# Kernel optimization log

Measured on AMD Instinct MI355X. Metric: run time of the kernel, lower is better.

Reference implementation:

```python
import jax, jax.numpy as jnp
import numpy as np

NUM_HEADS = 16
D_MODEL = 1024
DEPTH = D_MODEL // NUM_HEADS
THRESHOLD = 0.1
BATCH = 2
SEQ = 2048


def setup_inputs() -> dict:
    key = jax.random.key(0)
    ks = jax.random.split(key, 9)
    w_scale = 1.0 / np.sqrt(D_MODEL)
    Q = jax.random.normal(ks[0], (BATCH, SEQ, D_MODEL), dtype=jnp.float32)
    T = jax.random.normal(ks[1], (BATCH, SEQ, D_MODEL), dtype=jnp.float32)
    V = jax.random.normal(ks[2], (BATCH, SEQ, D_MODEL), dtype=jnp.float32)
    Wq = jax.random.normal(ks[3], (NUM_HEADS, D_MODEL, DEPTH), dtype=jnp.float32) * w_scale
    Wk = jax.random.normal(ks[4], (NUM_HEADS, D_MODEL, DEPTH), dtype=jnp.float32) * w_scale
    Wv = jax.random.normal(ks[5], (NUM_HEADS, D_MODEL, DEPTH), dtype=jnp.float32) * w_scale
    Wo = jax.random.normal(ks[6], (D_MODEL, D_MODEL), dtype=jnp.float32) * w_scale
    bq = jnp.zeros((NUM_HEADS, DEPTH), dtype=jnp.float32)
    bk = jnp.zeros((NUM_HEADS, DEPTH), dtype=jnp.float32)
    bv = jnp.zeros((NUM_HEADS, DEPTH), dtype=jnp.float32)
    bo = jnp.zeros((D_MODEL,), dtype=jnp.float32)
    return {"Q": Q, "T": T, "V": V, "Wq": Wq, "bq": bq, "Wk": Wk, "bk": bk,
            "Wv": Wv, "bv": bv, "Wo": Wo, "bo": bo}


def reference(Q, T, V, Wq, bq, Wk, bk, Wv, bv, Wo, bo):
    # Per-head projections (stacked over heads): [B,S,D] x [H,D,E] -> [B,H,S,E]
    q = jnp.einsum('bsd,hde->bhse', Q, Wq) + bq[None, :, None, :]
    k = jnp.einsum('bsd,hde->bhse', T, Wk) + bk[None, :, None, :]
    v = jnp.einsum('bsd,hde->bhse', V, Wv) + bv[None, :, None, :]

    # Raw scores (NOT pre-scaled): [B,H,S,S]
    scores = jnp.einsum('bhqe,bhke->bhqk', q, k)
    # tf.where(A>thr, A, -2**32 * cast(A>thr)) -> failing entries become 0
    scores = jnp.where(scores > THRESHOLD, scores, jnp.zeros((), scores.dtype))
    # M = 1 - lower_band(ones): +1 on strictly upper-triangular entries
    seq = scores.shape[-1]
    upper = jnp.triu(jnp.ones((seq, seq), dtype=scores.dtype), k=1)
    scores = (scores + upper) / jnp.sqrt(jnp.asarray(DEPTH, scores.dtype))

    attn = jax.nn.softmax(scores, axis=-1)
    out = jnp.einsum('bhqk,bhke->bhqe', attn, v)  # [B,H,S,E]
    B, H, S, E = out.shape
    concat = out.transpose(0, 2, 1, 3).reshape(B, S, H * E)  # [B,S,D]
    return concat @ Wo + bo
```

## Files before the change

### kernel.cpp

```cpp
#include <hip/hip_runtime.h>
#include <stdint.h>


typedef __attribute__((ext_vector_type(8))) short bf16x8;
typedef __attribute__((ext_vector_type(4))) float f32x4;

#define DEVFN static __device__ __forceinline__

static constexpr int S_ = 2048;
static constexpr int H_ = 16;

DEVFN unsigned short f2bf(float x) {
  union { float f; uint32_t u; } v; v.f = x;
  const uint32_t r = v.u + 0x7fffu + ((v.u >> 16) & 1u);
  return (unsigned short)(r >> 16);
}

DEVFN f32x4 fzero() { f32x4 v = {0.f, 0.f, 0.f, 0.f}; return v; }

union U8 { uint32_t u[4]; bf16x8 v; };

DEVFN void gld_lds16(const void* g, void* lds) {
  __builtin_amdgcn_global_load_lds(
      (const __attribute__((address_space(1))) void*)g,
      (__attribute__((address_space(3))) void*)lds, 16, 0, 0);
}

__global__ void prep_weights(const float* __restrict__ Wq, const float* __restrict__ Wk,
                             const float* __restrict__ Wv, const float* __restrict__ Wo,
                             unsigned short* __restrict__ dstBase) {
  const int z = blockIdx.z;
  const float* src = (z == 0) ? Wq : (z == 1) ? Wk : (z == 2) ? Wv : Wo;
  unsigned short* dst = dstBase + (size_t)z * (1024u * 1024u);
  const int idx = blockIdx.x * 256 + threadIdx.x;
  const int c = idx & 1023;
  const int d0 = (idx >> 10) << 3;
  unsigned short hv[8];
#pragma unroll
  for (int t = 0; t < 8; ++t) {
    const int d = d0 + t;
    const float v = (z < 3) ? src[(size_t)((c >> 6) * 1024 + d) * 64 + (c & 63)]
                            : src[(size_t)d * 1024 + c];
    hv[t] = f2bf(v);
  }
  *(uint4*)(dst + (size_t)c * 1024 + d0) = *(const uint4*)hv;
}

__global__ __launch_bounds__(256, 3)
void proj_gemm(const float* __restrict__ Qm, const float* __restrict__ Tm,
               const float* __restrict__ Vm, const unsigned short* __restrict__ Wt,
               const float* __restrict__ bq, const float* __restrict__ bk,
               const float* __restrict__ bv, unsigned short* __restrict__ qb,
               unsigned short* __restrict__ kb, unsigned short* __restrict__ vtb) {
  __shared__ float Af[2][128 * 32];
  __shared__ unsigned short Bt[2][128 * 32];

  const int tid = threadIdx.x;
  const int lane = tid & 63;
  const int w = tid >> 6;
  const int g = lane >> 4, c = lane & 15;
  const int wm = w >> 1, wn = w & 1;

  const int orig = blockIdx.x;
  const int xcd = orig & 7;
  const int l = orig >> 3;
  const int bx = xcd * 4 + l / 24;
  const int by = l % 24;

  const int m0 = bx * 128;
  const int proj = by >> 3;
  const int n0 = (by & 7) * 128;

  const float* Asrc = (proj == 0) ? Qm : (proj == 1) ? Tm : Vm;
  const unsigned short* W = Wt + (size_t)proj * (1024u * 1024u);

  f32x4 acc[4][4];
#pragma unroll
  for (int i = 0; i < 4; ++i)
#pragma unroll
    for (int j = 0; j < 4; ++j) acc[i][j] = fzero();

  const int arow = w * 8 + (lane >> 3);
  const int ach = lane & 7;
  const int brow = w * 16 + (lane >> 2);
  const int bch = lane & 3;

  auto stage = [&](int kt, int buf) {
#pragma unroll
    for (int u = 0; u < 4; ++u) {
      const int row = u * 32 + arow;
      const int ch = ach ^ (row & 7);
      gld_lds16(Asrc + (size_t)(m0 + row) * 1024 + kt * 32 + ch * 4,
                &Af[buf][(u * 32 + w * 8) * 32]);
    }
#pragma unroll
    for (int u = 0; u < 2; ++u) {
      const int row = u * 64 + brow;
      const int ch = bch ^ ((row >> 1) & 3);
      gld_lds16(W + (size_t)(n0 + row) * 1024 + kt * 32 + ch * 8,
                &Bt[buf][(u * 64 + w * 16) * 32]);
    }
  };

  stage(0, 0);
  __syncthreads();

  for (int kt = 0; kt < 32; ++kt) {
    const int buf = kt & 1;
    if (kt < 31) stage(kt + 1, buf ^ 1);

    bf16x8 af[4], bfr[4];
#pragma unroll
    for (int mi = 0; mi < 4; ++mi) {
      const int row = wm * 64 + mi * 16 + c;
      const int swz = row & 7;
      const float4 fa = *(const float4*)&Af[buf][row * 32 + ((2 * g) ^ swz) * 4];
      const float4 fb = *(const float4*)&Af[buf][row * 32 + ((2 * g + 1) ^ swz) * 4];
      U8 u8;
      asm("v_cvt_pk_bf16_f32 %0, %1, %2" : "=v"(u8.u[0]) : "v"(fa.x), "v"(fa.y));
      asm("v_cvt_pk_bf16_f32 %0, %1, %2" : "=v"(u8.u[1]) : "v"(fa.z), "v"(fa.w));
      asm("v_cvt_pk_bf16_f32 %0, %1, %2" : "=v"(u8.u[2]) : "v"(fb.x), "v"(fb.y));
      asm("v_cvt_pk_bf16_f32 %0, %1, %2" : "=v"(u8.u[3]) : "v"(fb.z), "v"(fb.w));
      af[mi] = u8.v;
    }
#pragma unroll
    for (int ni = 0; ni < 4; ++ni) {
      const int row = wn * 64 + ni * 16 + c;
      bfr[ni] = *(const bf16x8*)&Bt[buf][row * 32 + ((g ^ ((row >> 1) & 3))) * 8];
    }
#pragma unroll
    for (int mi = 0; mi < 4; ++mi)
#pragma unroll
      for (int ni = 0; ni < 4; ++ni)
        acc[mi][ni] = __builtin_amdgcn_mfma_f32_16x16x32_bf16(af[mi], bfr[ni],
                                                              acc[mi][ni], 0, 0, 0);
    __syncthreads();
  }

  const float* bias = (proj == 0) ? bq : (proj == 1) ? bk : bv;
  if (proj < 2) {
    unsigned short* dptr = (proj == 0) ? qb : kb;
#pragma unroll
    for (int ni = 0; ni < 4; ++ni) {
      const int colb = n0 + wn * 64 + ni * 16 + c;
      const float bc = bias[colb];
      const int hh = colb >> 6, e = colb & 63;
#pragma unroll
      for (int mi = 0; mi < 4; ++mi)
#pragma unroll
        for (int r = 0; r < 4; ++r) {
          const int row = m0 + wm * 64 + mi * 16 + g * 4 + r;
          const int bb = row >> 11, s = row & 2047;
          dptr[(((size_t)(bb * H_ + hh)) * S_ + s) * 64 + e] = f2bf(acc[mi][ni][r] + bc);
        }
    }
  } else {
#pragma unroll
    for (int ni = 0; ni < 4; ++ni) {
      const int colb = n0 + wn * 64 + ni * 16 + c;
      const float bc = bias[colb];
      const int hh = colb >> 6, e = colb & 63;
#pragma unroll
      for (int mi = 0; mi < 4; ++mi) {
        const int rowb = m0 + wm * 64 + mi * 16 + g * 4;
        const int bb = rowb >> 11, s0 = rowb & 2047;
        const float v0 = acc[mi][ni][0] + bc, v1 = acc[mi][ni][1] + bc;
        const float v2 = acc[mi][ni][2] + bc, v3 = acc[mi][ni][3] + bc;
        uint2 pk;
        asm("v_cvt_pk_bf16_f32 %0, %1, %2" : "=v"(pk.x) : "v"(v0), "v"(v1));
        asm("v_cvt_pk_bf16_f32 %0, %1, %2" : "=v"(pk.y) : "v"(v2), "v"(v3));
        *(uint2*)&vtb[(((size_t)(bb * H_ + hh)) * 64 + e) * S_ + s0] = pk;
      }
    }
  }
}

__global__ __launch_bounds__(256, 2)
void attn_kernel(const unsigned short* __restrict__ qb,
                 const unsigned short* __restrict__ kb,
                 const unsigned short* __restrict__ vtb,
                 unsigned short* __restrict__ att) {
  __shared__ unsigned short Kt[2][128 * 64];
  __shared__ unsigned short Vt[2][64 * 128];
  __shared__ unsigned short Pt[4][32 * 64];

  const int tid = threadIdx.x;
  const int lane = tid & 63;
  const int w = tid >> 6;
  const int g = lane >> 4, c = lane & 15;

  const int orig = blockIdx.x;
  const int logical = ((orig & 7) << 6) | (orig >> 3);
  const int qblk = logical & 15;
  const int bh = logical >> 4;
  const int hh = bh & 15, bz = bh >> 4;

  const int q0w = qblk * 128 + w * 32;
  const unsigned short* qh = qb + (size_t)bh * S_ * 64;
  const unsigned short* kh = kb + (size_t)bh * S_ * 64;
  const unsigned short* vh = vtb + (size_t)bh * 64 * S_;

  bf16x8 aq[2][2];
#pragma unroll
  for (int m = 0; m < 2; ++m)
#pragma unroll
    for (int t = 0; t < 2; ++t)
      aq[m][t] = *(const bf16x8*)&qh[(size_t)(q0w + m * 16 + c) * 64 + t * 32 + g * 8];

  bf16x8 onesB;
#pragma unroll
  for (int i = 0; i < 8; ++i) onesB[i] = (short)0x3F80;

  f32x4 O[2][4];
  f32x4 accL[2];
#pragma unroll
  for (int m = 0; m < 2; ++m) {
#pragma unroll
    for (int ne = 0; ne < 4; ++ne) O[m][ne] = fzero();
    accL[m] = fzero();
  }

  constexpr float L2E = 1.4426950408889634f;
  const float S2 = 0.125f * L2E;
  const float B2 = 0.125f * L2E;

  int kaOff[2][4];
  int vOff[2][2][4];
  int paOff[2][2], pwOff[2][4];
#pragma unroll
  for (int ks = 0; ks < 2; ++ks) {
#pragma unroll
    for (int mi = 0; mi < 4; ++mi) {
      const int row = mi * 16 + c;
      kaOff[ks][mi] = 2 * (row * 64 + ((ks * 4 + g) ^ (row & 7)) * 8);
    }
#pragma unroll
    for (int m = 0; m < 2; ++m)
      paOff[m][ks] = 2 * ((m * 16 + c) * 64 + ((ks * 4 + g) ^ (c & 7)) * 8);
  }
#pragma unroll
  for (int s = 0; s < 2; ++s)
#pragma unroll
    for (int ks = 0; ks < 2; ++ks)
#pragma unroll
      for (int ne = 0; ne < 4; ++ne) {
        const int e = ne * 16 + c;
        vOff[s][ks][ne] = 2 * (e * 128 + ((s * 8 + ks * 4 + g) ^ c) * 8);
      }
#pragma unroll
  for (int m = 0; m < 2; ++m)
#pragma unroll
    for (int mi = 0; mi < 4; ++mi)
      pwOff[m][mi] =
          2 * ((m * 16 + c) * 64 + ((2 * mi + (g >> 1)) ^ (c & 7)) * 8 + (g & 1) * 4);

  const int srowK = w * 8 + (lane >> 3);
  const int schK = (lane & 7) ^ (srowK & 7);
  const unsigned short* kS = kh + (size_t)srowK * 64 + schK * 8;
  const int rowV = w * 4 + (lane >> 4);
  const int jV = (lane & 15) ^ rowV;
  const unsigned short* vS = vh + (size_t)rowV * S_ + jV * 8;

  {
#pragma unroll
    for (int u = 0; u < 4; ++u) {
      gld_lds16(kS + u * 2048, &Kt[0][(u * 32 + w * 8) * 64]);
      gld_lds16(vS + (size_t)u * 32768, &Vt[0][(u * 16 + w * 4) * 128]);
    }
  }
  __syncthreads();

#define ATTN_SUB(J0S, SB, CUR)                                                 \
  do {                                                                         \
    const int j0 = (J0S);                                                      \
    f32x4 sa[2][4];                                                            \
    _Pragma("unroll")                                                          \
    for (int m = 0; m < 2; ++m)                                                \
      _Pragma("unroll")                                                        \
      for (int mi = 0; mi < 4; ++mi) sa[m][mi] = fzero();                      \
    __builtin_amdgcn_s_setprio(1);                                             \
    _Pragma("unroll")                                                          \
    for (int ks = 0; ks < 2; ++ks)                                             \
      _Pragma("unroll")                                                        \
      for (int mi = 0; mi < 4; ++mi) {                                         \
        const bf16x8 ka = *(const bf16x8*)((const char*)&Kt[CUR][0] +          \
                                           (SB) * 8192 + kaOff[ks][mi]);       \
        sa[0][mi] = __builtin_amdgcn_mfma_f32_16x16x32_bf16(ka, aq[0][ks],     \
                                                            sa[0][mi], 0, 0, 0);\
        sa[1][mi] = __builtin_amdgcn_mfma_f32_16x16x32_bf16(ka, aq[1][ks],     \
                                                            sa[1][mi], 0, 0, 0);\
      }                                                                        \
    __builtin_amdgcn_s_setprio(0);                                             \
    const bool allUp = (j0 >= q0w + 32);                                       \
    const bool noneUp = (j0 + 63 <= q0w);                                      \
    _Pragma("unroll")                                                          \
    for (int m = 0; m < 2; ++m) {                                              \
      const int iq = q0w + m * 16 + c;                                         \
      _Pragma("unroll")                                                        \
      for (int mi = 0; mi < 4; ++mi) {                                         \
        float pv[4];                                                           \
        if (allUp || noneUp) {                                                 \
          const float bb = allUp ? B2 : 0.f;                                   \
          _Pragma("unroll")                                                    \
          for (int r = 0; r < 4; ++r) {                                        \
            const float v = sa[m][mi][r];                                      \
            pv[r] = __builtin_amdgcn_exp2f(                                    \
                (v > 0.1f) ? __builtin_fmaf(v, S2, bb) : bb);                  \
          }                                                                    \
        } else {                                                               \
          _Pragma("unroll")                                                    \
          for (int r = 0; r < 4; ++r) {                                        \
            const float v = sa[m][mi][r];                                      \
            const float bb = (j0 + mi * 16 + g * 4 + r > iq) ? B2 : 0.f;       \
            pv[r] = __builtin_amdgcn_exp2f(                                    \
                (v > 0.1f) ? __builtin_fmaf(v, S2, bb) : bb);                  \
          }                                                                    \
        }                                                                      \
        uint2 d;                                                               \
        asm("v_cvt_pk_bf16_f32 %0, %1, %2"                                     \
            : "=v"(d.x) : "v"(pv[0]), "v"(pv[1]));                             \
        asm("v_cvt_pk_bf16_f32 %0, %1, %2"                                     \
            : "=v"(d.y) : "v"(pv[2]), "v"(pv[3]));                             \
        *(uint2*)((char*)&Pt[w][0] + pwOff[m][mi]) = d;                        \
      }                                                                        \
    }                                                                          \
    asm volatile("s_waitcnt lgkmcnt(0)" ::: "memory");                         \
    __builtin_amdgcn_sched_barrier(0);                                         \
    __builtin_amdgcn_s_setprio(1);                                             \
    _Pragma("unroll")                                                          \
    for (int ks = 0; ks < 2; ++ks) {                                           \
      const bf16x8 pa0 =                                                       \
          *(const bf16x8*)((const char*)&Pt[w][0] + paOff[0][ks]);             \
      const bf16x8 pa1 =                                                       \
          *(const bf16x8*)((const char*)&Pt[w][0] + paOff[1][ks]);             \
      accL[0] = __builtin_amdgcn_mfma_f32_16x16x32_bf16(pa0, onesB, accL[0],   \
                                                        0, 0, 0);              \
      accL[1] = __builtin_amdgcn_mfma_f32_16x16x32_bf16(pa1, onesB, accL[1],   \
                                                        0, 0, 0);              \
      _Pragma("unroll")                                                        \
      for (int ne = 0; ne < 4; ++ne) {                                         \
        const bf16x8 bv8 = *(const bf16x8*)((const char*)&Vt[CUR][0] +         \
                                            vOff[SB][ks][ne]);                 \
        O[0][ne] = __builtin_amdgcn_mfma_f32_16x16x32_bf16(pa0, bv8, O[0][ne], \
                                                           0, 0, 0);           \
        O[1][ne] = __builtin_amdgcn_mfma_f32_16x16x32_bf16(pa1, bv8, O[1][ne], \
                                                           0, 0, 0);           \
      }                                                                        \
    }                                                                          \
    __builtin_amdgcn_s_setprio(0);                                             \
  } while (0)

#define ATTN_TILE(T, CUR)                                                      \
  do {                                                                         \
    if ((T) < 15) {       \
      _Pragma("unroll")                                                        \
      for (int u = 0; u < 4; ++u) {                                            \
        gld_lds16(kS + 8192 + u * 2048, &Kt[CUR ^ 1][(u * 32 + w * 8) * 64]);  \
        gld_lds16(vS + 128 + (size_t)u * 32768,                                \
                  &Vt[CUR ^ 1][(u * 16 + w * 4) * 128]);                       \
      }                                                                        \
      kS += 8192; vS += 128;                                                   \
    }                                                                          \
    ATTN_SUB((T) * 128, 0, CUR);                                               \
    ATTN_SUB((T) * 128 + 64, 1, CUR);                                          \
    __syncthreads();         \
  } while (0)

  for (int T = 0; T < 16; T += 2) {
    ATTN_TILE(T, 0);
    ATTN_TILE(T + 1, 1);
  }
#undef ATTN_TILE
#undef ATTN_SUB

#pragma unroll
  for (int m = 0; m < 2; ++m)
#pragma unroll
    for (int r = 0; r < 4; ++r) {
      const float il = 1.f / accL[m][r];
      const int qg = q0w + m * 16 + g * 4 + r;
      const size_t ro = ((size_t)(bz * S_ + qg)) * 1024 + hh * 64;
#pragma unroll
      for (int ne = 0; ne < 4; ++ne)
        att[ro + ne * 16 + c] = f2bf(O[m][ne][r] * il);
    }
}

__global__ __launch_bounds__(256, 3)
void out_gemm(const unsigned short* __restrict__ att,
              const unsigned short* __restrict__ WoT,
              const float* __restrict__ bo, float* __restrict__ outp) {
  __shared__ unsigned short At[2][128 * 32];
  __shared__ unsigned short Bt[2][128 * 32];

  const int tid = threadIdx.x;
  const int lane = tid & 63;
  const int w = tid >> 6;
  const int g = lane >> 4, c = lane & 15;
  const int wm = w >> 1, wn = w & 1;

  const int orig = blockIdx.x;
  const int xcd = orig & 7;
  const int l = orig >> 3;
  const int bx = xcd * 4 + l / 8;
  const int by = l % 8;
  const int m0 = bx * 128;
  const int n0 = by * 128;

  f32x4 acc[4][4];
#pragma unroll
  for (int i = 0; i < 4; ++i)
#pragma unroll
    for (int j = 0; j < 4; ++j) acc[i][j] = fzero();

  const int srow = lane >> 2;
  const int sch = lane & 3;

  auto stage = [&](int kt, int buf) {
#pragma unroll
    for (int u = 0; u < 2; ++u) {
      const int row = u * 64 + w * 16 + srow;
      const int ch = sch ^ ((row >> 1) & 3);
      gld_lds16(att + (size_t)(m0 + row) * 1024 + kt * 32 + ch * 8,
                &At[buf][(u * 64 + w * 16) * 32]);
      gld_lds16(WoT + (size_t)(n0 + row) * 1024 + kt * 32 + ch * 8,
                &Bt[buf][(u * 64 + w * 16) * 32]);
    }
  };

  stage(0, 0);
  __syncthreads();

  for (int kt = 0; kt < 32; ++kt) {
    const int buf = kt & 1;
    if (kt < 31) stage(kt + 1, buf ^ 1);

    bf16x8 af[4], bfr[4];
#pragma unroll
    for (int mi = 0; mi < 4; ++mi) {
      const int row = wm * 64 + mi * 16 + c;
      af[mi] = *(const bf16x8*)&At[buf][row * 32 + ((g ^ ((row >> 1) & 3))) * 8];
    }
#pragma unroll
    for (int ni = 0; ni < 4; ++ni) {
      const int row = wn * 64 + ni * 16 + c;
      bfr[ni] = *(const bf16x8*)&Bt[buf][row * 32 + ((g ^ ((row >> 1) & 3))) * 8];
    }
#pragma unroll
    for (int mi = 0; mi < 4; ++mi)
#pragma unroll
      for (int ni = 0; ni < 4; ++ni)
        acc[mi][ni] = __builtin_amdgcn_mfma_f32_16x16x32_bf16(af[mi], bfr[ni],
                                                              acc[mi][ni], 0, 0, 0);
    __syncthreads();
  }

#pragma unroll
  for (int ni = 0; ni < 4; ++ni) {
    const int colb = n0 + wn * 64 + ni * 16 + c;
    const float bc = bo[colb];
#pragma unroll
    for (int mi = 0; mi < 4; ++mi)
#pragma unroll
      for (int r = 0; r < 4; ++r) {
        const int row = m0 + wm * 64 + mi * 16 + g * 4 + r;
        outp[(size_t)row * 1024 + colb] = acc[mi][ni][r] + bc;
      }
  }
}

extern "C" void kernel_launch(void* const* d_in, const int* in_sizes, int n_in,
                              void* d_out, int out_size, void* d_ws, size_t ws_size,
                              hipStream_t stream) {
  const float* Q  = (const float*)d_in[0];
  const float* T  = (const float*)d_in[1];
  const float* V  = (const float*)d_in[2];
  const float* Wq = (const float*)d_in[3];
  const float* bq = (const float*)d_in[4];
  const float* Wk = (const float*)d_in[5];
  const float* bk = (const float*)d_in[6];
  const float* Wv = (const float*)d_in[7];
  const float* bv = (const float*)d_in[8];
  const float* Wo = (const float*)d_in[9];
  const float* bo = (const float*)d_in[10];

  const size_t MB = 1024ull * 1024ull;
  if (ws_size < 40 * MB) return;

  uint8_t* ws = (uint8_t*)d_ws;
  unsigned short* Wt  = (unsigned short*)(ws);
  unsigned short* qb  = (unsigned short*)(ws + 8 * MB);
  unsigned short* kb  = (unsigned short*)(ws + 16 * MB);
  unsigned short* vtb = (unsigned short*)(ws + 24 * MB);
  unsigned short* attb = (unsigned short*)(ws + 32 * MB);

  prep_weights<<<dim3(512, 1, 4), 256, 0, stream>>>(Wq, Wk, Wv, Wo, Wt);
  proj_gemm<<<dim3(768), 256, 0, stream>>>(Q, T, V, Wt, bq, bk, bv,
                                           qb, kb, vtb);
  attn_kernel<<<dim3(512), 256, 0, stream>>>(qb, kb, vtb, attb);
  out_gemm<<<dim3(256), 256, 0, stream>>>(attb, Wt + 3ull * 1024ull * 1024ull,
                                          bo, (float*)d_out);
}
```

Before: 131.5 us.

## Pre-convert projection activations to bf16 in a separate kernel before GEMM

New measurement: 138.3 us. +5.2%, slower.

```diff
diff --git a/kernel.cpp b/kernel.cpp
--- a/kernel.cpp
+++ b/kernel.cpp
@@ -17,8 +17,6 @@
 }
 
 DEVFN f32x4 fzero() { f32x4 v = {0.f, 0.f, 0.f, 0.f}; return v; }
-
-union U8 { uint32_t u[4]; bf16x8 v; };
 
 DEVFN void gld_lds16(const void* g, void* lds) {
   __builtin_amdgcn_global_load_lds(
@@ -46,13 +44,39 @@
   *(uint4*)(dst + (size_t)c * 1024 + d0) = *(const uint4*)hv;
 }
 
-__global__ __launch_bounds__(256, 3)
-void proj_gemm(const float* __restrict__ Qm, const float* __restrict__ Tm,
-               const float* __restrict__ Vm, const unsigned short* __restrict__ Wt,
+__global__ void convert_a(const float* __restrict__ Qm, const float* __restrict__ Tm,
+                          const float* __restrict__ Vm, unsigned short* __restrict__ aq,
+                          unsigned short* __restrict__ at2, unsigned short* __restrict__ av) {
+  const int z = blockIdx.z;
+  const float* s = (z == 0) ? Qm : (z == 1) ? Tm : Vm;
+  unsigned short* d = (z == 0) ? aq : (z == 1) ? at2 : av;
+  const int orig = blockIdx.x;
+  const int xcd = orig & 7;
+  const int j = orig >> 3;
+  const int p = xcd * 4 + (j >> 6);
+  const int inner = j & 63;
+  const size_t i = (size_t)p * 131072 + (size_t)inner * 2048 +
+                   (size_t)threadIdx.x * 8;
+  const float4 f0 = *(const float4*)(s + i);
+  const float4 f1 = *(const float4*)(s + i + 4);
+  uint32_t d0, d1, d2, d3;
+  asm("v_cvt_pk_bf16_f32 %0, %1, %2" : "=v"(d0) : "v"(f0.x), "v"(f0.y));
+  asm("v_cvt_pk_bf16_f32 %0, %1, %2" : "=v"(d1) : "v"(f0.z), "v"(f0.w));
+  asm("v_cvt_pk_bf16_f32 %0, %1, %2" : "=v"(d2) : "v"(f1.x), "v"(f1.y));
+  asm("v_cvt_pk_bf16_f32 %0, %1, %2" : "=v"(d3) : "v"(f1.z), "v"(f1.w));
+  uint4 o; o.x = d0; o.y = d1; o.z = d2; o.w = d3;
+  *(uint4*)(d + i) = o;
+}
+
+__global__ __launch_bounds__(256, 4)
+void proj_gemm(const unsigned short* __restrict__ Aq,
+               const unsigned short* __restrict__ At2,
+               const unsigned short* __restrict__ Av,
+               const unsigned short* __restrict__ Wt,
                const float* __restrict__ bq, const float* __restrict__ bk,
                const float* __restrict__ bv, unsigned short* __restrict__ qb,
                unsigned short* __restrict__ kb, unsigned short* __restrict__ vtb) {
-  __shared__ float Af[2][128 * 32];
+  __shared__ unsigned short At[2][128 * 32];
   __shared__ unsigned short Bt[2][128 * 32];
 
   const int tid = threadIdx.x;
@@ -71,7 +95,7 @@
   const int proj = by >> 3;
   const int n0 = (by & 7) * 128;
 
-  const float* Asrc = (proj == 0) ? Qm : (proj == 1) ? Tm : Vm;
+  const unsigned short* Abf = (proj == 0) ? Aq : (proj == 1) ? At2 : Av;
   const unsigned short* W = Wt + (size_t)proj * (1024u * 1024u);
 
   f32x4 acc[4][4];
@@ -80,23 +104,16 @@
 #pragma unroll
     for (int j = 0; j < 4; ++j) acc[i][j] = fzero();
 
-  const int arow = w * 8 + (lane >> 3);
-  const int ach = lane & 7;
-  const int brow = w * 16 + (lane >> 2);
-  const int bch = lane & 3;
+  const int srow = lane >> 2;
+  const int sch = lane & 3;
 
   auto stage = [&](int kt, int buf) {
 #pragma unroll
-    for (int u = 0; u < 4; ++u) {
-      const int row = u * 32 + arow;
-      const int ch = ach ^ (row & 7);
-      gld_lds16(Asrc + (size_t)(m0 + row) * 1024 + kt * 32 + ch * 4,
-                &Af[buf][(u * 32 + w * 8) * 32]);
-    }
-#pragma unroll
     for (int u = 0; u < 2; ++u) {
-      const int row = u * 64 + brow;
-      const int ch = bch ^ ((row >> 1) & 3);
+      const int row = u * 64 + w * 16 + srow;
+      const int ch = sch ^ ((row >> 1) & 3);
+      gld_lds16(Abf + (size_t)(m0 + row) * 1024 + kt * 32 + ch * 8,
+                &At[buf][(u * 64 + w * 16) * 32]);
       gld_lds16(W + (size_t)(n0 + row) * 1024 + kt * 32 + ch * 8,
                 &Bt[buf][(u * 64 + w * 16) * 32]);
     }
@@ -113,27 +130,21 @@
 #pragma unroll
     for (int mi = 0; mi < 4; ++mi) {
       const int row = wm * 64 + mi * 16 + c;
-      const int swz = row & 7;
-      const float4 fa = *(const float4*)&Af[buf][row * 32 + ((2 * g) ^ swz) * 4];
-      const float4 fb = *(const float4*)&Af[buf][row * 32 + ((2 * g + 1) ^ swz) * 4];
-      U8 u8;
-      asm("v_cvt_pk_bf16_f32 %0, %1, %2" : "=v"(u8.u[0]) : "v"(fa.x), "v"(fa.y));
-      asm("v_cvt_pk_bf16_f32 %0, %1, %2" : "=v"(u8.u[1]) : "v"(fa.z), "v"(fa.w));
-      asm("v_cvt_pk_bf16_f32 %0, %1, %2" : "=v"(u8.u[2]) : "v"(fb.x), "v"(fb.y));
-      asm("v_cvt_pk_bf16_f32 %0, %1, %2" : "=v"(u8.u[3]) : "v"(fb.z), "v"(fb.w));
-      af[mi] = u8.v;
+      af[mi] = *(const bf16x8*)&At[buf][row * 32 + ((g ^ ((row >> 1) & 3))) * 8];
     }
 #pragma unroll
     for (int ni = 0; ni < 4; ++ni) {
       const int row = wn * 64 + ni * 16 + c;
       bfr[ni] = *(const bf16x8*)&Bt[buf][row * 32 + ((g ^ ((row >> 1) & 3))) * 8];
     }
+    __builtin_amdgcn_s_setprio(1);
 #pragma unroll
     for (int mi = 0; mi < 4; ++mi)
 #pragma unroll
       for (int ni = 0; ni < 4; ++ni)
         acc[mi][ni] = __builtin_amdgcn_mfma_f32_16x16x32_bf16(af[mi], bfr[ni],
                                                               acc[mi][ni], 0, 0, 0);
+    __builtin_amdgcn_s_setprio(0);
     __syncthreads();
   }
 
@@ -352,7 +363,7 @@
 
 #define ATTN_TILE(T, CUR)                                                      \
   do {                                                                         \
-    if ((T) < 15) {       \
+    if ((T) < 15) {                                                            \
       _Pragma("unroll")                                                        \
       for (int u = 0; u < 4; ++u) {                                            \
         gld_lds16(kS + 8192 + u * 2048, &Kt[CUR ^ 1][(u * 32 + w * 8) * 64]);  \
@@ -363,7 +374,7 @@
     }                                                                          \
     ATTN_SUB((T) * 128, 0, CUR);                                               \
     ATTN_SUB((T) * 128 + 64, 1, CUR);                                          \
-    __syncthreads();         \
+    __syncthreads();                                                           \
   } while (0)
 
   for (int T = 0; T < 16; T += 2) {
@@ -494,8 +505,13 @@
   unsigned short* vtb = (unsigned short*)(ws + 24 * MB);
   unsigned short* attb = (unsigned short*)(ws + 32 * MB);
 
+  unsigned short* aQ = (unsigned short*)d_out;
+  unsigned short* aT = aQ + 4ull * 1024ull * 1024ull;
+  unsigned short* aV = attb;
+
   prep_weights<<<dim3(512, 1, 4), 256, 0, stream>>>(Wq, Wk, Wv, Wo, Wt);
-  proj_gemm<<<dim3(768), 256, 0, stream>>>(Q, T, V, Wt, bq, bk, bv,
+  convert_a<<<dim3(2048, 1, 3), 256, 0, stream>>>(Q, T, V, aQ, aT, aV);
+  proj_gemm<<<dim3(768), 256, 0, stream>>>(aQ, aT, aV, Wt, bq, bk, bv,
                                            qb, kb, vtb);
   attn_kernel<<<dim3(512), 256, 0, stream>>>(qb, kb, vtb, attb);
   out_gemm<<<dim3(256), 256, 0, stream>>>(attb, Wt + 3ull * 1024ull * 1024ull,
```
